# Optimization experiments

Measured on AMD Instinct MI355X. Metric: run time of the kernel, lower is better.

Reference implementation:

```python
import jax, jax.numpy as jnp
import numpy as np

T, B, I, H, P, O = 512, 256, 64, 128, 256, 50
NUM_LAYERS = 2
BN_EPS = 1e-5


def _gru_scan(xs, h0, Wih, Whh, bih, bhh):
    # xs: [T, B, in]; precompute input projections for all steps at once
    xp = jnp.einsum('tbi,gi->tbg', xs, Wih) + bih  # [T, B, 3H]

    def step(h, x_t):
        gh = h @ Whh.T + bhh                      # [B, 3H]
        xr, xz, xn = jnp.split(x_t, 3, axis=-1)
        hr, hz, hn = jnp.split(gh, 3, axis=-1)
        r = jax.nn.sigmoid(xr + hr)
        z = jax.nn.sigmoid(xz + hz)
        n = jnp.tanh(xn + r * hn)
        h_new = (1.0 - z) * n + z * h
        return h_new, h_new

    _, ys = jax.lax.scan(step, h0, xp)
    return ys  # [T, B, H]


def setup_inputs() -> dict:
    key = jax.random.key(0)
    ks = jax.random.split(key, 24)
    s = 0.05
    inp = {
        'x': jax.random.normal(ks[0], (T, B, I), dtype=jnp.float32),
        'h0': jnp.zeros((NUM_LAYERS, B, H), dtype=jnp.float32),
        # GRU layer 0 (input I -> H)
        'Wih0': jax.random.normal(ks[1], (3 * H, I)) * s,
        'Whh0': jax.random.normal(ks[2], (3 * H, H)) * s,
        'bih0': jax.random.normal(ks[3], (3 * H,)) * s,
        'bhh0': jax.random.normal(ks[4], (3 * H,)) * s,
        # GRU layer 1 (input H -> H)
        'Wih1': jax.random.normal(ks[5], (3 * H, H)) * s,
        'Whh1': jax.random.normal(ks[6], (3 * H, H)) * s,
        'bih1': jax.random.normal(ks[7], (3 * H,)) * s,
        'bhh1': jax.random.normal(ks[8], (3 * H,)) * s,
        # proj Linear H -> P
        'Wp': jax.random.normal(ks[9], (P, H)) * s,
        'bp': jax.random.normal(ks[10], (P,)) * s,
        # BatchNorm1d(P) affine params (training-mode batch stats)
        'gamma': jnp.ones((P,), dtype=jnp.float32),
        'beta': jnp.zeros((P,), dtype=jnp.float32),
        # GRUCell P -> P
        'Wcih': jax.random.normal(ks[11], (3 * P, P)) * s,
        'Wchh': jax.random.normal(ks[12], (3 * P, P)) * s,
        'bcih': jax.random.normal(ks[13], (3 * P,)) * s,
        'bchh': jax.random.normal(ks[14], (3 * P,)) * s,
        # input skip Linear I -> P
        'Ws': jax.random.normal(ks[15], (P, I)) * s,
        'bs': jax.random.normal(ks[16], (P,)) * s,
        # final Linear P -> O
        'Wf': jax.random.normal(ks[17], (O, P)) * s,
        'bf': jax.random.normal(ks[18], (O,)) * s,
    }
    return inp


def reference(x, h0, Wih0, Whh0, bih0, bhh0, Wih1, Whh1, bih1, bhh1,
              Wp, bp, gamma, beta, Wcih, Wchh, bcih, bchh, Ws, bs, Wf, bf):
    # two-layer unidirectional GRU
    y0 = _gru_scan(x, h0[0], Wih0, Whh0, bih0, bhh0)   # [T, B, H]
    rnn_out = _gru_scan(y0, h0[1], Wih1, Whh1, bih1, bhh1)  # [T, B, H]

    # linear projection to proj_dim
    proj_seq = jnp.einsum('tbh,ph->tbp', rnn_out, Wp) + bp  # [T, B, P]

    # BatchNorm1d in training mode over flattened (batch*time), per-feature
    mean = jnp.mean(proj_seq, axis=(0, 1))
    var = jnp.mean((proj_seq - mean) ** 2, axis=(0, 1))  # biased variance
    bn_seq = gamma * (proj_seq - mean) * jax.lax.rsqrt(var + BN_EPS) + beta

    # sequential GRUCell refinement over time, GELU on each step's state
    cell_h0 = jnp.zeros((x.shape[1], Wchh.shape[1]), dtype=bn_seq.dtype)
    cell_states = _gru_scan(bn_seq, cell_h0, Wcih, Wchh, bcih, bchh)  # [T, B, P]
    refined_seq = jax.nn.gelu(cell_states, approximate=False)

    # residual skip from raw input
    skip_seq = jnp.einsum('tbi,pi->tbp', x, Ws) + bs

    aggregated = jnp.mean(refined_seq + skip_seq, axis=0)  # [B, P]
    out = aggregated @ Wf.T + bf                            # [B, O]
    return out
```

## Files before the change

kernel.cpp:

```cpp
#include <hip/hip_runtime.h>

#define T_DIM 512
#define B_DIM 256
#define I_DIM 64
#define H_DIM 128
#define P_DIM 256
#define O_DIM 50

typedef _Float16 half8 __attribute__((ext_vector_type(8)));
typedef _Float16 half4 __attribute__((ext_vector_type(4)));
typedef float f32x4 __attribute__((ext_vector_type(4)));

#define GLOAD_LDS16(G, L)                                                      \
  __builtin_amdgcn_global_load_lds(                                            \
      (const __attribute__((address_space(1))) void*)(G),                      \
      (__attribute__((address_space(3))) void*)(L), 16, 0, 0)

__device__ __forceinline__ float sigm(float x) {
  return __builtin_amdgcn_rcpf(1.f + __expf(-x));
}
__device__ __forceinline__ float tanh_f(float x) {
  x = fminf(20.f, fmaxf(-20.f, x));
  float e = __expf(2.f * x);
  return (e - 1.f) * __builtin_amdgcn_rcpf(e + 1.f);
}

__global__ void cvt_k(const float* __restrict__ s, _Float16* __restrict__ d, long n) {
  long i = (long)blockIdx.x * blockDim.x + threadIdx.x;
  long st = (long)gridDim.x * blockDim.x;
  for (; i < n; i += st) d[i] = (_Float16)s[i];
}

__global__ void xmean_k(const float* __restrict__ x, float* __restrict__ xm) {
  int b = blockIdx.x, i = threadIdx.x;
  float s = 0.f;
  for (int t = 0; t < T_DIM; ++t) s += x[((long)t * B_DIM + b) * I_DIM + i];
  xm[b * I_DIM + i] = s * (1.0f / T_DIM);
}

__global__ void skip_k(const float* __restrict__ xm, const float* __restrict__ Wsk,
                       const float* __restrict__ bsk, float* __restrict__ skipm) {
  int b = blockIdx.x, p = threadIdx.x;
  float s = bsk[p];
  for (int i = 0; i < I_DIM; ++i) s += xm[b * I_DIM + i] * Wsk[p * I_DIM + i];
  skipm[b * P_DIM + p] = s;
}

__global__ void zero2_k(float* a, float* b2) {
  int p = threadIdx.x;
  a[p] = 0.f;
  b2[p] = 0.f;
}

__global__ void zeroN_k(float* a, int n) {
  int i = blockIdx.x * blockDim.x + threadIdx.x;
  if (i < n) a[i] = 0.f;
}

__global__ void bnprep_k(const float* gsum, const float* gss, const float* gamma,
                         const float* beta, float* bns, float* bnt) {
  int p = threadIdx.x;
  const float inv = 1.0f / ((float)T_DIM * (float)B_DIM);
  float m = gsum[p] * inv;
  float v = gss[p] * inv - m * m;
  float rs = rsqrtf(v + 1e-5f);
  float s = gamma[p] * rs;
  bns[p] = s;
  bnt[p] = beta[p] - m * s;
}

__global__ void fold_k(const float* __restrict__ Wcih, const float* __restrict__ bcih,
                       const float* __restrict__ bns, const float* __restrict__ bnt,
                       _Float16* __restrict__ WF, float* __restrict__ bF) {
  __shared__ float red[256];
  int n = blockIdx.x, k = threadIdx.x;
  float wv = Wcih[n * 256 + k];
  WF[n * 256 + k] = (_Float16)(wv * bns[k]);
  red[k] = wv * bnt[k];
  __syncthreads();
  for (int s = 128; s > 0; s >>= 1) {
    if (k < s) red[k] += red[k + s];
    __syncthreads();
  }
  if (k == 0) bF[n] = bcih[n] + red[0];
}

__global__ __launch_bounds__(256) void gemm_k(
    const _Float16* __restrict__ A, const _Float16* __restrict__ W,
    const float* __restrict__ bias, const float* __restrict__ bias2, int n2lim,
    _Float16* __restrict__ C, int M, int N, int K, int transN,
    float* __restrict__ gsum, float* __restrict__ gss) {
  __shared__ __align__(16) _Float16 As[128 * 64];
  __shared__ __align__(16) _Float16 Bs[128 * 64];
  const int tid = threadIdx.x;
  const int l = tid & 63;
  const int w = tid >> 6;
  const int wr = w >> 1, wc = w & 1;
  const int lrow = l & 15, lk = l >> 4;
  const long bm = blockIdx.x, bn = blockIdx.y;

  f32x4 z = {0.f, 0.f, 0.f, 0.f};
  f32x4 acc[4][4];
#pragma unroll
  for (int m = 0; m < 4; ++m)
#pragma unroll
    for (int n = 0; n < 4; ++n) acc[m][n] = z;

  for (int k0 = 0; k0 < K; k0 += 64) {
    if (k0) __syncthreads();
#pragma unroll
    for (int it = 0; it < 4; ++it) {
      const int lin = it * 256 + tid;
      const int row = lin >> 3, slot = lin & 7;
      const int scol = (slot ^ (row & 7)) << 3;
      GLOAD_LDS16(A + (bm * 128 + row) * (long)K + k0 + scol, (_Float16*)As + (size_t)lin * 8);
      GLOAD_LDS16(W + (bn * 128 + row) * (long)K + k0 + scol, (_Float16*)Bs + (size_t)lin * 8);
    }
    __syncthreads();
#pragma unroll
    for (int kk = 0; kk < 2; ++kk) {
      half8 af[4], wfr[4];
#pragma unroll
      for (int m = 0; m < 4; ++m) {
        const int row = wr * 64 + m * 16 + lrow;
        af[m] = *(const half8*)((const char*)As +
                                ((row * 128 + (kk * 32 + lk * 8) * 2) ^ ((row & 7) << 4)));
      }
#pragma unroll
      for (int n = 0; n < 4; ++n) {
        const int row = wc * 64 + n * 16 + lrow;
        wfr[n] = *(const half8*)((const char*)Bs +
                                 ((row * 128 + (kk * 32 + lk * 8) * 2) ^ ((row & 7) << 4)));
      }
#pragma unroll
      for (int m = 0; m < 4; ++m)
#pragma unroll
        for (int n = 0; n < 4; ++n)
          acc[m][n] = __builtin_amdgcn_mfma_f32_16x16x32_f16(af[m], wfr[n], acc[m][n], 0, 0, 0);
    }
  }
  if (transN) {
    const long tIdx = bm >> 1;
    const long TCH = M >> 8;
#pragma unroll
    for (int n = 0; n < 4; ++n) {
      const int gn = (int)bn * 128 + wc * 64 + n * 16 + lrow;
      float bv = 0.f;
      if (bias) bv += bias[gn];
      if (bias2 && gn < n2lim) bv += bias2[gn];
#pragma unroll
      for (int m = 0; m < 4; ++m) {
        half4 v;
#pragma unroll
        for (int r = 0; r < 4; ++r) v[r] = (_Float16)(acc[m][n][r] + bv);
        const int blk = (int)(bm & 1) * 8 + wr * 4 + m;
        *(half4*)(C + ((blk * TCH + tIdx) * N + gn) * 16 + lk * 4) = v;
      }
    }
  } else {
#pragma unroll
    for (int n = 0; n < 4; ++n) {
      const int gn = (int)bn * 128 + wc * 64 + n * 16 + lrow;
      float bv = 0.f;
      if (bias) bv += bias[gn];
      if (bias2 && gn < n2lim) bv += bias2[gn];
      float sm = 0.f, sq = 0.f;
#pragma unroll
      for (int m = 0; m < 4; ++m)
#pragma unroll
        for (int r = 0; r < 4; ++r) {
          const long gm = bm * 128 + wr * 64 + m * 16 + lk * 4 + r;
          _Float16 pv = (_Float16)(acc[m][n][r] + bv);
          C[gm * (long)N + gn] = pv;
          float pf = (float)pv;
          sm += pf;
          sq += pf * pf;
        }
      if (gsum) {
        sm += __shfl_xor(sm, 16);
        sm += __shfl_xor(sm, 32);
        sq += __shfl_xor(sq, 16);
        sq += __shfl_xor(sq, 32);
        if (lk == 0) {
          atomicAdd(&gsum[gn], sm);
          atomicAdd(&gss[gn], sq);
        }
      }
    }
  }
}

__global__ __launch_bounds__(512, 1) void scan01_pipe(
    const _Float16* __restrict__ xp0T,
    const _Float16* __restrict__ Whh0h,
    const _Float16* __restrict__ Wih1h,
    const _Float16* __restrict__ Whh1h,
    const float* __restrict__ bhh0, const float* __restrict__ bih1,
    const float* __restrict__ bhh1,
    const float* __restrict__ h0init,
    _Float16* __restrict__ y0buf,
    _Float16* __restrict__ h1buf,
    int* flags) {
  __shared__ __align__(16) _Float16 hL[2][16 * 128];
  const int tid = threadIdx.x;
  const int l = tid & 63, w = tid >> 6;
  const int lrow = l & 15, lk = l >> 4;
  const int bblk = blockIdx.x & 15;
  const int rbase = bblk * 16;
  const int p = w * 16 + lrow;

  if (blockIdx.x < 16) {
    half8 wf0[3][4];
#pragma unroll
    for (int g = 0; g < 3; ++g)
#pragma unroll
      for (int kk = 0; kk < 4; ++kk)
        wf0[g][kk] = *(const half8*)(Whh0h + (size_t)(g * 128 + p) * 128 + kk * 32 + lk * 8);
    const float bN0 = bhh0[2 * H_DIM + p];
    float h0r[4];
#pragma unroll
    for (int r = 0; r < 4; ++r) h0r[r] = h0init[(rbase + lk * 4 + r) * H_DIM + p];
    for (int i = tid; i < 16 * 128; i += 512) {
      int row = i >> 7, pp = i & 127;
      int byte = (row * 256 + pp * 2) ^ ((row & 7) << 4);
      *(_Float16*)((char*)hL[1] + byte) = (_Float16)h0init[(rbase + row) * H_DIM + pp];
    }
    __syncthreads();

    half4 xA[3], xB[3];
    auto loadx = [&](half4(&X)[3], int tt) {
#pragma unroll
      for (int g = 0; g < 3; ++g)
        X[g] = *(const half4*)(xp0T + (((long)bblk * T_DIM + tt) * 384 + g * 128 + p) * 16 +
                               lk * 4);
    };
    auto pstep = [&](int t, half4(&XC)[3], half4(&XN)[3]) {
      loadx(XN, (t + 1 < T_DIM) ? t + 1 : T_DIM - 1);
      char* cur = (char*)hL[(t & 1) ^ 1];
      char* nxt = (char*)hL[t & 1];
      half8 af[4];
#pragma unroll
      for (int kk = 0; kk < 4; ++kk) {
        int byte = (lrow * 256 + (kk * 32 + lk * 8) * 2) ^ ((lrow & 7) << 4);
        af[kk] = *(const half8*)(cur + byte);
      }
      f32x4 aR, aZ, aN;
#pragma unroll
      for (int r = 0; r < 4; ++r) {
        aR[r] = (float)XC[0][r];
        aZ[r] = (float)XC[1][r];
        aN[r] = 0.f;
      }
#pragma unroll
      for (int kk = 0; kk < 4; ++kk) {
        aR = __builtin_amdgcn_mfma_f32_16x16x32_f16(af[kk], wf0[0][kk], aR, 0, 0, 0);
        aZ = __builtin_amdgcn_mfma_f32_16x16x32_f16(af[kk], wf0[1][kk], aZ, 0, 0, 0);
        aN = __builtin_amdgcn_mfma_f32_16x16x32_f16(af[kk], wf0[2][kk], aN, 0, 0, 0);
      }
#pragma unroll
      for (int r = 0; r < 4; ++r) {
        float rg = sigm(aR[r]);
        float zg = sigm(aZ[r]);
        float ng = tanh_f((float)XC[2][r] + rg * (aN[r] + bN0));
        float hv = ng + zg * (h0r[r] - ng);
        h0r[r] = hv;
        int row = lk * 4 + r;
        int byte = (row * 256 + p * 2) ^ ((row & 7) << 4);
        *(_Float16*)(nxt + byte) = (_Float16)hv;
        y0buf[((size_t)(bblk * T_DIM + t) * 16 + row) * 128 + p] = (_Float16)hv;
      }
      if ((t & 3) == 3) {
        __threadfence();
        __syncthreads();
        if (tid == 0)
          __hip_atomic_store(&flags[bblk], t + 1, __ATOMIC_RELEASE, __HIP_MEMORY_SCOPE_AGENT);
      } else {
        __syncthreads();
      }
    };
    loadx(xA, 0);
    for (int t = 0; t < T_DIM; t += 2) {
      pstep(t, xA, xB);
      pstep(t + 1, xB, xA);
    }
  } else {
    half8 wf1x[3][4], wf1h[3][4];
#pragma unroll
    for (int g = 0; g < 3; ++g)
#pragma unroll
      for (int kk = 0; kk < 4; ++kk) {
        const size_t ro = (size_t)(g * 128 + p) * 128 + kk * 32 + lk * 8;
        wf1x[g][kk] = *(const half8*)(Wih1h + ro);
        wf1h[g][kk] = *(const half8*)(Whh1h + ro);
      }
    const float bR1 = bih1[p] + bhh1[p];
    const float bZ1 = bih1[H_DIM + p] + bhh1[H_DIM + p];
    const float bX1 = bih1[2 * H_DIM + p];
    const float bN1 = bhh1[2 * H_DIM + p];
    float h1r[4];
#pragma unroll
    for (int r = 0; r < 4; ++r)
      h1r[r] = h0init[B_DIM * H_DIM + (rbase + lk * 4 + r) * H_DIM + p];
    for (int i = tid; i < 16 * 128; i += 512) {
      int row = i >> 7, pp = i & 127;
      int byte = (row * 256 + pp * 2) ^ ((row & 7) << 4);
      *(_Float16*)((char*)hL[1] + byte) =
          (_Float16)h0init[B_DIM * H_DIM + (rbase + row) * H_DIM + pp];
    }
    __syncthreads();

    const _Float16* yb = y0buf + (size_t)bblk * T_DIM * 16 * 128;
    int avail = 0;
    auto wait_for = [&](int target) {
      if (avail < target) {
        do {
          __builtin_amdgcn_s_sleep(2);
          avail = __hip_atomic_load(&flags[bblk], __ATOMIC_ACQUIRE, __HIP_MEMORY_SCOPE_AGENT);
        } while (avail < target);
      }
    };
    auto loady = [&](half8(&Y)[4], int tt) {
#pragma unroll
      for (int kk = 0; kk < 4; ++kk)
        Y[kk] = *(const half8*)(yb + ((size_t)tt * 16 + lrow) * 128 + kk * 32 + lk * 8);
    };
    auto cstep = [&](int t, half8(&YC)[4], half8(&YN)[4]) {
      wait_for((t + 2 < T_DIM) ? (t + 2) : T_DIM);
      loady(YN, (t + 1 < T_DIM) ? t + 1 : T_DIM - 1);
      char* cur = (char*)hL[(t & 1) ^ 1];
      char* nxt = (char*)hL[t & 1];
      f32x4 aRx = {bR1, bR1, bR1, bR1};
      f32x4 aZx = {bZ1, bZ1, bZ1, bZ1};
      f32x4 aX = {bX1, bX1, bX1, bX1};
      f32x4 aRh = {0.f, 0.f, 0.f, 0.f};
      f32x4 aZh = {0.f, 0.f, 0.f, 0.f};
      f32x4 aH = {0.f, 0.f, 0.f, 0.f};
      half8 ah[4];
#pragma unroll
      for (int kk = 0; kk < 4; ++kk) {
        int byte = (lrow * 256 + (kk * 32 + lk * 8) * 2) ^ ((lrow & 7) << 4);
        ah[kk] = *(const half8*)(cur + byte);
      }
#pragma unroll
      for (int kk = 0; kk < 4; ++kk) {
        aRx = __builtin_amdgcn_mfma_f32_16x16x32_f16(YC[kk], wf1x[0][kk], aRx, 0, 0, 0);
        aZx = __builtin_amdgcn_mfma_f32_16x16x32_f16(YC[kk], wf1x[1][kk], aZx, 0, 0, 0);
        aX = __builtin_amdgcn_mfma_f32_16x16x32_f16(YC[kk], wf1x[2][kk], aX, 0, 0, 0);
        aRh = __builtin_amdgcn_mfma_f32_16x16x32_f16(ah[kk], wf1h[0][kk], aRh, 0, 0, 0);
        aZh = __builtin_amdgcn_mfma_f32_16x16x32_f16(ah[kk], wf1h[1][kk], aZh, 0, 0, 0);
        aH = __builtin_amdgcn_mfma_f32_16x16x32_f16(ah[kk], wf1h[2][kk], aH, 0, 0, 0);
      }
#pragma unroll
      for (int r = 0; r < 4; ++r) {
        float rg = sigm(aRx[r] + aRh[r]);
        float zg = sigm(aZx[r] + aZh[r]);
        float ng = tanh_f(aX[r] + rg * (aH[r] + bN1));
        float hv = ng + zg * (h1r[r] - ng);
        h1r[r] = hv;
        int row = lk * 4 + r;
        int byte = (row * 256 + p * 2) ^ ((row & 7) << 4);
        *(_Float16*)(nxt + byte) = (_Float16)hv;
        h1buf[((long)t * B_DIM + rbase + row) * 128 + p] = (_Float16)hv;
      }
      __syncthreads();
    };
    half8 yA[4], yB[4];
    wait_for(2);
    loady(yA, 0);
    for (int t = 0; t < T_DIM; t += 2) {
      cstep(t, yA, yB);
      cstep(t + 1, yB, yA);
    }
  }
}

__global__ __launch_bounds__(512, 1) void scan_cell(
    const _Float16* __restrict__ xpT,
    _Float16* __restrict__ hT,
    float* __restrict__ hst, const _Float16* __restrict__ Whh,
    const float* __restrict__ bhh, int TC, int first) {
  __shared__ __align__(16) _Float16 hL[2][16 * 256];
  __shared__ __align__(16) _Float16 WL[768 * 64];
  const int tid = threadIdx.x;
  const int l = tid & 63, w = tid >> 6;
  const int lrow = l & 15, lk = l >> 4;
  const int rbase = blockIdx.x * 16;

  half8 wf[6][6];
#pragma unroll
  for (int g = 0; g < 3; ++g)
#pragma unroll
    for (int c = 0; c < 2; ++c) {
      const int nt = g * 16 + 2 * w + c;
#pragma unroll
      for (int kk = 0; kk < 6; ++kk)
        wf[g * 2 + c][kk] =
            *(const half8*)(Whh + (size_t)(nt * 16 + lrow) * P_DIM + kk * 32 + lk * 8);
    }
  for (int q = tid; q < 768 * 8; q += 512) {
    int row = q >> 3, slot = q & 7;
    int scol = (slot ^ (row & 7)) << 3;
    *(half8*)((char*)WL + (size_t)q * 16) = *(const half8*)(Whh + (size_t)row * P_DIM + 192 + scol);
  }
  float bN[2];
#pragma unroll
  for (int c = 0; c < 2; ++c) bN[c] = bhh[2 * P_DIM + 32 * w + 16 * c + lrow];

  float h[2][4];
#pragma unroll
  for (int c = 0; c < 2; ++c)
#pragma unroll
    for (int r = 0; r < 4; ++r)
      h[c][r] = first ? 0.f : hst[(rbase + lk * 4 + r) * P_DIM + 32 * w + 16 * c + lrow];
  for (int i = tid; i < 16 * 256; i += 512) {
    int row = i >> 8, pp = i & 255;
    float hv = first ? 0.f : hst[(rbase + row) * P_DIM + pp];
    int byte = (row * 512 + pp * 2) ^ ((row & 7) << 4);
    *(_Float16*)((char*)hL[0] + byte) = (_Float16)hv;
  }
  __syncthreads();

  half4 xA[3][2], xB[3][2];
  auto loadx = [&](half4(&X)[3][2], int tt) {
#pragma unroll
    for (int g = 0; g < 3; ++g)
#pragma unroll
      for (int c = 0; c < 2; ++c)
        X[g][c] = *(const half4*)(xpT +
                                  (((long)blockIdx.x * TC + tt) * 768 + g * 256 + 32 * w + 16 * c +
                                   lrow) * 16 + lk * 4);
  };
  auto step = [&](int tt, half4(&XC)[3][2], half4(&XN)[3][2], int tn) {
    loadx(XN, tn);
    char* hCur = (char*)hL[tt & 1];
    char* hNxt = (char*)hL[(tt & 1) ^ 1];
    half8 af[4];
    f32x4 acc[3][2];
#pragma unroll
    for (int c = 0; c < 2; ++c)
#pragma unroll
      for (int r = 0; r < 4; ++r) {
        acc[0][c][r] = (float)XC[0][c][r];
        acc[1][c][r] = (float)XC[1][c][r];
        acc[2][c][r] = 0.f;
      }
#pragma unroll
    for (int kk = 0; kk < 4; ++kk) {
      int byte = (lrow * 512 + (kk * 32 + lk * 8) * 2) ^ ((lrow & 7) << 4);
      af[kk] = *(const half8*)(hCur + byte);
    }
#pragma unroll
    for (int g = 0; g < 3; ++g)
#pragma unroll
      for (int c = 0; c < 2; ++c)
#pragma unroll
        for (int kk = 0; kk < 4; ++kk)
          acc[g][c] =
              __builtin_amdgcn_mfma_f32_16x16x32_f16(af[kk], wf[g * 2 + c][kk], acc[g][c], 0, 0, 0);
#pragma unroll
    for (int kk = 0; kk < 4; ++kk) {
      int byte = (lrow * 512 + ((kk + 4) * 32 + lk * 8) * 2) ^ ((lrow & 7) << 4);
      af[kk] = *(const half8*)(hCur + byte);
    }
#pragma unroll
    for (int g = 0; g < 3; ++g)
#pragma unroll
      for (int c = 0; c < 2; ++c) {
        const int nt = g * 16 + 2 * w + c;
        const int wrow = nt * 16 + lrow;
        f32x4 a = acc[g][c];
        a = __builtin_amdgcn_mfma_f32_16x16x32_f16(af[0], wf[g * 2 + c][4], a, 0, 0, 0);
        a = __builtin_amdgcn_mfma_f32_16x16x32_f16(af[1], wf[g * 2 + c][5], a, 0, 0, 0);
        half8 w6 = *(const half8*)((char*)WL + ((wrow * 128 + lk * 16) ^ ((wrow & 7) << 4)));
        half8 w7 = *(const half8*)((char*)WL + ((wrow * 128 + 64 + lk * 16) ^ ((wrow & 7) << 4)));
        a = __builtin_amdgcn_mfma_f32_16x16x32_f16(af[2], w6, a, 0, 0, 0);
        a = __builtin_amdgcn_mfma_f32_16x16x32_f16(af[3], w7, a, 0, 0, 0);
        acc[g][c] = a;
      }
#pragma unroll
    for (int c = 0; c < 2; ++c) {
      half4 hv4;
#pragma unroll
      for (int r = 0; r < 4; ++r) {
        float rg = sigm(acc[0][c][r]);
        float zg = sigm(acc[1][c][r]);
        float ng = tanh_f((float)XC[2][c][r] + rg * (acc[2][c][r] + bN[c]));
        float hv = ng + zg * (h[c][r] - ng);
        h[c][r] = hv;
        hv4[r] = (_Float16)hv;
        const int row = lk * 4 + r, pp = 32 * w + 16 * c + lrow;
        int byte = (row * 512 + pp * 2) ^ ((row & 7) << 4);
        *(_Float16*)(hNxt + byte) = hv4[r];
      }
      *(half4*)(hT + ((long)tt * 256 + 32 * w + 16 * c + lrow) * 256 + rbase + lk * 4) = hv4;
    }
    __syncthreads();
  };
  loadx(xA, 0);
  for (int t = 0; t < TC; t += 2) {
    step(t, xA, xB, t + 1);
    step(t + 1, xB, xA, (t + 2 < TC) ? t + 2 : TC - 1);
  }
#pragma unroll
  for (int c = 0; c < 2; ++c)
#pragma unroll
    for (int r = 0; r < 4; ++r)
      hst[(rbase + lk * 4 + r) * P_DIM + 32 * w + 16 * c + lrow] = h[c][r];
}

__global__ void gelu_mean_k(const _Float16* __restrict__ hT, float* __restrict__ aggT) {
  int p = blockIdx.x, b = threadIdx.x;
  int t0 = blockIdx.y * 64;
  float s = 0.f;
  for (int t = t0; t < t0 + 64; ++t) {
    float v = (float)hT[((long)t * P_DIM + p) * B_DIM + b];
    s += 0.5f * v * (1.f + erff(v * 0.70710678118f));
  }
  atomicAdd(&aggT[p * B_DIM + b], s);
}

__global__ void final_k(const float* __restrict__ aggT, const float* __restrict__ skipm,
                        const float* __restrict__ Wf, const float* __restrict__ bfb,
                        float* __restrict__ out) {
  int b = blockIdx.x, o = threadIdx.x;
  if (o >= O_DIM) return;
  float s = bfb[o];
  for (int p = 0; p < P_DIM; ++p)
    s += (aggT[p * B_DIM + b] * (1.0f / T_DIM) + skipm[b * P_DIM + p]) * Wf[o * P_DIM + p];
  out[b * O_DIM + o] = s;
}

extern "C" void kernel_launch(void* const* d_in, const int* in_sizes, int n_in, void* d_out,
                              int out_size, void* d_ws, size_t ws_size, hipStream_t stream) {
  const float* x = (const float*)d_in[0];
  const float* h0 = (const float*)d_in[1];
  const float* Wih0 = (const float*)d_in[2];
  const float* Whh0f = (const float*)d_in[3];
  const float* bih0 = (const float*)d_in[4];
  const float* bhh0 = (const float*)d_in[5];
  const float* Wih1 = (const float*)d_in[6];
  const float* Whh1f = (const float*)d_in[7];
  const float* bih1 = (const float*)d_in[8];
  const float* bhh1 = (const float*)d_in[9];
  const float* Wp = (const float*)d_in[10];
  const float* bp = (const float*)d_in[11];
  const float* gamma = (const float*)d_in[12];
  const float* beta = (const float*)d_in[13];
  const float* Wcih = (const float*)d_in[14];
  const float* Wchhf = (const float*)d_in[15];
  const float* bcih = (const float*)d_in[16];
  const float* bchh = (const float*)d_in[17];
  const float* Wsk = (const float*)d_in[18];
  const float* bsk = (const float*)d_in[19];
  const float* Wf = (const float*)d_in[20];
  const float* bfb = (const float*)d_in[21];
  float* out = (float*)d_out;

  char* wsp = (char*)d_ws;
  size_t off = 0;
  auto alloc = [&](size_t b) -> void* {
    void* p = wsp + off;
    off = (off + b + 255) & ~(size_t)255;
    return p;
  };
  _Float16* xh = (_Float16*)alloc((size_t)T_DIM * B_DIM * I_DIM * 2);
  _Float16* wih0 = (_Float16*)alloc(384 * 64 * 2);
  _Float16* whh0 = (_Float16*)alloc(384 * 128 * 2);
  _Float16* wih1 = (_Float16*)alloc(384 * 128 * 2);
  _Float16* whh1 = (_Float16*)alloc(384 * 128 * 2);
  _Float16* wp = (_Float16*)alloc(256 * 128 * 2);
  _Float16* wcihF = (_Float16*)alloc(768 * 256 * 2);
  _Float16* wchh = (_Float16*)alloc(768 * 256 * 2);
  _Float16* proj = (_Float16*)alloc((size_t)T_DIM * B_DIM * P_DIM * 2);
  _Float16* hT = (_Float16*)alloc((size_t)T_DIM * B_DIM * P_DIM * 2);
  float* hstc = (float*)alloc(B_DIM * P_DIM * 4);
  float* aggT = (float*)alloc(B_DIM * P_DIM * 4);
  float* xm = (float*)alloc(B_DIM * I_DIM * 4);
  float* skipm = (float*)alloc(B_DIM * P_DIM * 4);
  float* gsum = (float*)alloc(256 * 4);
  float* gss = (float*)alloc(256 * 4);
  float* bns = (float*)alloc(256 * 4);
  float* bnt = (float*)alloc(256 * 4);
  float* bcihF = (float*)alloc(768 * 4);
  int* flags = (int*)alloc(64 * 4);

  _Float16* y0buf = proj;
  _Float16* h1buf = hT;

  const size_t xp0_bytes = (size_t)T_DIM * 384 * B_DIM * 2;
  int TC2 = 512;
  while (TC2 > 32 && off + ((size_t)TC2 * B_DIM * 768 * 2 > xp0_bytes
                                ? (size_t)TC2 * B_DIM * 768 * 2
                                : xp0_bytes) >
                         ws_size)
    TC2 >>= 1;
  size_t xpb_bytes = (size_t)TC2 * B_DIM * 768 * 2;
  if (xpb_bytes < xp0_bytes) xpb_bytes = xp0_bytes;
  _Float16* xpb = (_Float16*)alloc(xpb_bytes);
  const int nc2 = T_DIM / TC2;
  const int M2 = TC2 * B_DIM;

  auto cvt = [&](const float* s, _Float16* d, long n) {
    long g = (n + 255) / 256;
    if (g > 2048) g = 2048;
    cvt_k<<<dim3((unsigned)g), dim3(256), 0, stream>>>(s, d, n);
  };
  cvt(x, xh, (long)T_DIM * B_DIM * I_DIM);
  cvt(Wih0, wih0, 384 * 64);
  cvt(Whh0f, whh0, 384 * 128);
  cvt(Wih1, wih1, 384 * 128);
  cvt(Whh1f, whh1, 384 * 128);
  cvt(Wp, wp, 256 * 128);
  cvt(Wchhf, wchh, 768 * 256);

  xmean_k<<<B_DIM, I_DIM, 0, stream>>>(x, xm);
  skip_k<<<B_DIM, P_DIM, 0, stream>>>(xm, Wsk, bsk, skipm);
  zero2_k<<<1, 256, 0, stream>>>(gsum, gss);
  zeroN_k<<<256, 256, 0, stream>>>(aggT, B_DIM * P_DIM);
  zeroN_k<<<1, 64, 0, stream>>>((float*)flags, 64);

  gemm_k<<<dim3(T_DIM * B_DIM / 128, 3), 256, 0, stream>>>(
      xh, wih0, bih0, bhh0, 2 * H_DIM, xpb, T_DIM * B_DIM, 3 * H_DIM, I_DIM, 1, nullptr, nullptr);
  scan01_pipe<<<32, 512, 0, stream>>>(xpb, whh0, wih1, whh1, bhh0, bih1, bhh1, h0, y0buf, h1buf,
                                      flags);
  gemm_k<<<dim3(T_DIM * B_DIM / 128, 2), 256, 0, stream>>>(
      h1buf, wp, bp, (const float*)nullptr, 0, proj, T_DIM * B_DIM, P_DIM, H_DIM, 0, gsum, gss);
  bnprep_k<<<1, 256, 0, stream>>>(gsum, gss, gamma, beta, bns, bnt);
  fold_k<<<768, 256, 0, stream>>>(Wcih, bcih, bns, bnt, wcihF, bcihF);
  for (int c = 0; c < nc2; ++c) {
    const _Float16* pc = proj + (size_t)c * TC2 * B_DIM * P_DIM;
    gemm_k<<<dim3(M2 / 128, 6), 256, 0, stream>>>(pc, wcihF, bcihF, bchh, 2 * P_DIM, xpb, M2,
                                                  3 * P_DIM, P_DIM, 1, nullptr, nullptr);
    scan_cell<<<16, 512, 0, stream>>>(xpb, hT + (size_t)c * TC2 * B_DIM * P_DIM, hstc, wchh, bchh,
                                      TC2, c == 0);
  }
  gelu_mean_k<<<dim3(P_DIM, 8), B_DIM, 0, stream>>>(hT, aggT);
  final_k<<<B_DIM, 64, 0, stream>>>(aggT, skipm, Wf, bfb, out);
}
```

Before: 2.430 ms.

## Merge small setup kernels and publish layer-0 progress flag less often

Merges the six weight conversions into one multi-array conversion kernel. Fuses the time-mean of x with the skip projection into one kernel that splits the time reduction over four thread groups. Folds the BatchNorm statistics prep into fold_k, which removes a launch and two temporary buffers. Separately, the layer-0 producer in the pipelined scan now publishes its progress flag every 8 steps instead of every 4, trading fewer fences for coarser producer/consumer overlap.

```diff
diff --git a/kernel.cpp b/kernel.cpp
--- a/kernel.cpp
+++ b/kernel.cpp
@@ -31,19 +31,44 @@
   for (; i < n; i += st) d[i] = (_Float16)s[i];
 }
 
-__global__ void xmean_k(const float* __restrict__ x, float* __restrict__ xm) {
-  int b = blockIdx.x, i = threadIdx.x;
+__global__ void cvt6_k(const float* a0, _Float16* b0, int n0, const float* a1, _Float16* b1,
+                       int n1, const float* a2, _Float16* b2, int n2, const float* a3,
+                       _Float16* b3, int n3, const float* a4, _Float16* b4, int n4,
+                       const float* a5, _Float16* b5, int n5) {
+  int i = blockIdx.x * blockDim.x + threadIdx.x;
+  int st = gridDim.x * blockDim.x;
+  int total = n0 + n1 + n2 + n3 + n4 + n5;
+  for (; i < total; i += st) {
+    int j = i;
+    if (j < n0) { b0[j] = (_Float16)a0[j]; continue; }
+    j -= n0;
+    if (j < n1) { b1[j] = (_Float16)a1[j]; continue; }
+    j -= n1;
+    if (j < n2) { b2[j] = (_Float16)a2[j]; continue; }
+    j -= n2;
+    if (j < n3) { b3[j] = (_Float16)a3[j]; continue; }
+    j -= n3;
+    if (j < n4) { b4[j] = (_Float16)a4[j]; continue; }
+    j -= n4;
+    b5[j] = (_Float16)a5[j];
+  }
+}
+
+__global__ void xmean_skip_k(const float* __restrict__ x, const float* __restrict__ Wsk,
+                             const float* __restrict__ bsk, float* __restrict__ skipm) {
+  __shared__ float xs[4][64];
+  __shared__ float xmf[64];
+  const int b = blockIdx.x, tid = threadIdx.x;
+  const int i = tid & 63, q = tid >> 6;
   float s = 0.f;
-  for (int t = 0; t < T_DIM; ++t) s += x[((long)t * B_DIM + b) * I_DIM + i];
-  xm[b * I_DIM + i] = s * (1.0f / T_DIM);
-}
-
-__global__ void skip_k(const float* __restrict__ xm, const float* __restrict__ Wsk,
-                       const float* __restrict__ bsk, float* __restrict__ skipm) {
-  int b = blockIdx.x, p = threadIdx.x;
-  float s = bsk[p];
-  for (int i = 0; i < I_DIM; ++i) s += xm[b * I_DIM + i] * Wsk[p * I_DIM + i];
-  skipm[b * P_DIM + p] = s;
+  for (int t = q * 128; t < (q + 1) * 128; ++t) s += x[((long)t * B_DIM + b) * I_DIM + i];
+  xs[q][i] = s;
+  __syncthreads();
+  if (tid < 64) xmf[tid] = (xs[0][tid] + xs[1][tid] + xs[2][tid] + xs[3][tid]) * (1.0f / T_DIM);
+  __syncthreads();
+  float acc = bsk[tid];
+  for (int k = 0; k < I_DIM; ++k) acc += xmf[k] * Wsk[tid * I_DIM + k];
+  skipm[b * P_DIM + tid] = acc;
 }
 
 __global__ void zero2_k(float* a, float* b2) {
@@ -57,26 +82,21 @@
   if (i < n) a[i] = 0.f;
 }
 
-__global__ void bnprep_k(const float* gsum, const float* gss, const float* gamma,
-                         const float* beta, float* bns, float* bnt) {
-  int p = threadIdx.x;
-  const float inv = 1.0f / ((float)T_DIM * (float)B_DIM);
-  float m = gsum[p] * inv;
-  float v = gss[p] * inv - m * m;
-  float rs = rsqrtf(v + 1e-5f);
-  float s = gamma[p] * rs;
-  bns[p] = s;
-  bnt[p] = beta[p] - m * s;
-}
-
 __global__ void fold_k(const float* __restrict__ Wcih, const float* __restrict__ bcih,
-                       const float* __restrict__ bns, const float* __restrict__ bnt,
+                       const float* __restrict__ gsum, const float* __restrict__ gss,
+                       const float* __restrict__ gamma, const float* __restrict__ beta,
                        _Float16* __restrict__ WF, float* __restrict__ bF) {
   __shared__ float red[256];
   int n = blockIdx.x, k = threadIdx.x;
+  const float inv = 1.0f / ((float)T_DIM * (float)B_DIM);
+  float m = gsum[k] * inv;
+  float v = gss[k] * inv - m * m;
+  float rs = rsqrtf(v + 1e-5f);
+  float sc = gamma[k] * rs;
+  float tn = beta[k] - m * sc;
   float wv = Wcih[n * 256 + k];
-  WF[n * 256 + k] = (_Float16)(wv * bns[k]);
-  red[k] = wv * bnt[k];
+  WF[n * 256 + k] = (_Float16)(wv * sc);
+  red[k] = wv * tn;
   __syncthreads();
   for (int s = 128; s > 0; s >>= 1) {
     if (k < s) red[k] += red[k + s];
@@ -269,7 +289,7 @@
         *(_Float16*)(nxt + byte) = (_Float16)hv;
         y0buf[((size_t)(bblk * T_DIM + t) * 16 + row) * 128 + p] = (_Float16)hv;
       }
-      if ((t & 3) == 3) {
+      if ((t & 7) == 7) {
         __threadfence();
         __syncthreads();
         if (tid == 0)
@@ -575,12 +595,9 @@
   _Float16* hT = (_Float16*)alloc((size_t)T_DIM * B_DIM * P_DIM * 2);
   float* hstc = (float*)alloc(B_DIM * P_DIM * 4);
   float* aggT = (float*)alloc(B_DIM * P_DIM * 4);
-  float* xm = (float*)alloc(B_DIM * I_DIM * 4);
   float* skipm = (float*)alloc(B_DIM * P_DIM * 4);
   float* gsum = (float*)alloc(256 * 4);
   float* gss = (float*)alloc(256 * 4);
-  float* bns = (float*)alloc(256 * 4);
-  float* bnt = (float*)alloc(256 * 4);
   float* bcihF = (float*)alloc(768 * 4);
   int* flags = (int*)alloc(64 * 4);
 
@@ -600,21 +617,12 @@
   const int nc2 = T_DIM / TC2;
   const int M2 = TC2 * B_DIM;
 
-  auto cvt = [&](const float* s, _Float16* d, long n) {
-    long g = (n + 255) / 256;
-    if (g > 2048) g = 2048;
-    cvt_k<<<dim3((unsigned)g), dim3(256), 0, stream>>>(s, d, n);
-  };
-  cvt(x, xh, (long)T_DIM * B_DIM * I_DIM);
-  cvt(Wih0, wih0, 384 * 64);
-  cvt(Whh0f, whh0, 384 * 128);
-  cvt(Wih1, wih1, 384 * 128);
-  cvt(Whh1f, whh1, 384 * 128);
-  cvt(Wp, wp, 256 * 128);
-  cvt(Wchhf, wchh, 768 * 256);
-
-  xmean_k<<<B_DIM, I_DIM, 0, stream>>>(x, xm);
-  skip_k<<<B_DIM, P_DIM, 0, stream>>>(xm, Wsk, bsk, skipm);
+  cvt_k<<<dim3(2048), dim3(256), 0, stream>>>(x, xh, (long)T_DIM * B_DIM * I_DIM);
+  cvt6_k<<<dim3(512), dim3(256), 0, stream>>>(Wih0, wih0, 384 * 64, Whh0f, whh0, 384 * 128, Wih1,
+                                              wih1, 384 * 128, Whh1f, whh1, 384 * 128, Wp, wp,
+                                              256 * 128, Wchhf, wchh, 768 * 256);
+
+  xmean_skip_k<<<B_DIM, P_DIM, 0, stream>>>(x, Wsk, bsk, skipm);
   zero2_k<<<1, 256, 0, stream>>>(gsum, gss);
   zeroN_k<<<256, 256, 0, stream>>>(aggT, B_DIM * P_DIM);
   zeroN_k<<<1, 64, 0, stream>>>((float*)flags, 64);
@@ -625,8 +633,7 @@
                                       flags);
   gemm_k<<<dim3(T_DIM * B_DIM / 128, 2), 256, 0, stream>>>(
       h1buf, wp, bp, (const float*)nullptr, 0, proj, T_DIM * B_DIM, P_DIM, H_DIM, 0, gsum, gss);
-  bnprep_k<<<1, 256, 0, stream>>>(gsum, gss, gamma, beta, bns, bnt);
-  fold_k<<<768, 256, 0, stream>>>(Wcih, bcih, bns, bnt, wcihF, bcihF);
+  fold_k<<<768, 256, 0, stream>>>(Wcih, bcih, gsum, gss, gamma, beta, wcihF, bcihF);
   for (int c = 0; c < nc2; ++c) {
     const _Float16* pc = proj + (size_t)c * TC2 * B_DIM * P_DIM;
     gemm_k<<<dim3(M2 / 128, 6), 256, 0, stream>>>(pc, wcihF, bcihF, bchh, 2 * P_DIM, xpb, M2,
```

New measurement: 2.081 ms. 14.4% less time.
